# Kernel tuning notes

Hardware: AMD Instinct MI355X
Metric: run time of the kernel (lower is better)

The kernel has to match this reference:

```python
import jax, jax.numpy as jnp
import numpy as np

M, N, P, T = 8000, 63, 64, 5


def setup_inputs() -> dict:
    key = jax.random.key(0)
    ks = jax.random.split(key, 19)
    sn = (1.0 / N) ** 0.5
    sp = (1.0 / P) ** 0.5
    f32 = jnp.float32
    return {
        "A": jax.random.normal(ks[0], (1, M, N), f32),
        "b": jax.random.normal(ks[1], (1, M), f32),
        "c": jax.random.normal(ks[2], (1, N), f32),
        "theta1r": sn * jax.random.normal(ks[3], (P, N + 1), f32),
        "theta1c": sn * jax.random.normal(ks[4], (P, N + 1), f32),
        "theta2rr": sp * jax.random.normal(ks[5], (P, P), f32),
        "theta2rc": sp * jax.random.normal(ks[6], (P, P), f32),
        "theta2cr": sp * jax.random.normal(ks[7], (P, P), f32),
        "theta3rr": sp * jax.random.normal(ks[8], (P, P), f32),
        "theta3rc": sp * jax.random.normal(ks[9], (P, P), f32),
        "theta3cr": sp * jax.random.normal(ks[10], (P, P), f32),
        "theta4rr": sp * jax.random.normal(ks[11], (P,), f32),
        "theta4rc": sp * jax.random.normal(ks[12], (P,), f32),
        "theta4cr": sp * jax.random.normal(ks[13], (P,), f32),
        "theta6r": sp * jax.random.normal(ks[14], (P, P), f32),
        "theta6c": sp * jax.random.normal(ks[15], (P, P), f32),
        "theta7": sp * jax.random.normal(ks[16], (P, P), f32),
        "W8": 0.05 * jax.random.normal(ks[17], (2, 2 * P), f32),
        "b8": 0.05 * jax.random.normal(ks[18], (2,), f32),
        "z": 7,
    }


def reference(A, b, c, theta1r, theta1c, theta2rr, theta2rc, theta2cr,
              theta3rr, theta3rc, theta3cr, theta4rr, theta4rc, theta4cr,
              theta6r, theta6c, theta7, W8, b8, z):
    relu = jax.nn.relu
    m, n = A.shape[1], A.shape[2]
    p = theta1r.shape[0]
    # raw node features: row node v -> [A[v,:], b[v]]; column node m -> [c, 0]
    Fr_raw = jnp.concatenate([A[0], b[0][:, None]], axis=1)        # (m, n+1)
    fc_raw = jnp.concatenate([c[0], jnp.zeros((1,), A.dtype)])     # (n+1,)
    Fr = Fr_raw / jnp.linalg.norm(Fr_raw, axis=1, keepdims=True)   # f(v), v < m
    fc = fc_raw / jnp.linalg.norm(fc_raw)                          # f(m)
    # edge weights w(v,u) = f(v).f(u) are detached in the original (float(...data))
    Frd = jax.lax.stop_gradient(Fr)
    fcd = jax.lax.stop_gradient(fc)
    Wrr = Frd @ Frd.T                                              # (m, m)
    dg = jnp.diagonal(Wrr)
    srr_pos = relu(Wrr).sum(axis=1) - relu(dg)                     # sum over u != v
    srr_neg = relu(-Wrr).sum(axis=1) - relu(-dg)
    wrc = Frd @ fcd                                                # (m,) = w(v, m)
    # identity: sum_u relu(t4 * w_u) = relu(t4) * sum_u relu(w_u) + relu(-t4) * sum_u relu(-w_u)
    Srr = relu(theta4rr)[:, None] * srr_pos[None, :] + relu(-theta4rr)[:, None] * srr_neg[None, :]
    Src = relu(theta4rc)[:, None] * relu(wrc)[None, :] + relu(-theta4rc)[:, None] * relu(-wrc)[None, :]
    scr = relu(theta4cr) * relu(wrc).sum() + relu(-theta4cr) * relu(-wrc).sum()
    edge_r = theta3rr @ Srr + theta3rc @ Src                       # (p, m), constant over t
    edge_c = theta3cr @ scr                                        # (p,)
    fz = Fr[z]                                                     # z < m: row node feature
    t1r = theta1r @ fz                                             # (p,)
    t1c = theta1c @ fz
    # mu init (p, m+1) = [[Ab^T, c0^T]; 0]; split into row columns / column node
    mu_r0 = jnp.zeros((p, m), A.dtype).at[: n + 1].set(Fr_raw.T)
    mu_c0 = jnp.zeros((p,), A.dtype).at[: n + 1].set(fc_raw)

    def step(carry, _):
        mu_r, mu_c = carry
        # row nodes: term2rr uses old mu[:, v]; term2rc uses old mu[:, m]
        new_r = relu(t1r[:, None] + theta2rr @ mu_r + (theta2rc @ mu_c)[:, None] + edge_r)
        # column node updated last within a sweep -> sees updated row embeddings
        new_c = relu(t1c + theta2cr @ new_r.sum(axis=1) + edge_c)
        return (new_r, new_c), None

    (mu_r, mu_c), _ = jax.lax.scan(step, (mu_r0, mu_c0), None, length=T)
    term6 = theta6r @ mu_r.sum(axis=1) + theta6c @ mu_c            # (p,)
    term7 = theta7 @ mu_r[:, z]                                    # (p,)
    feat = jax.nn.sigmoid(jnp.concatenate([term6, term7]))         # (2p,)
    return (feat @ W8.T + b8)[None, :]                             # (1, 2)
```

## Files before the change

### kernel.cpp

```cpp
#include <hip/hip_runtime.h>
#include <math.h>

typedef __attribute__((ext_vector_type(8))) short short8;
typedef __attribute__((ext_vector_type(4))) float f32x4;

#define WS_SPART 0
#define WS_GPART 131072
#define WS_WPART 163840
#define WS_CPART 164864
#define WS_T1R   204864
#define WS_T1C   204928
#define WS_AL    204992
#define WS_BE    205056
#define WS_GA    205120
#define WS_DE    205184
#define WS_ECP   205248
#define WS_ECN   205312
#define WS_W     205376
#define WS_MUZ   205760
#define WS_WSUM  205824
#define WS_RNORM 205888
#define WS_R2H   214080
#define WS_R2L   216128
#define WS_E4    218176
#define WS_FH    250176
#define WS_FL    512320

__device__ __forceinline__ float waveReduceSum(float v) {
#pragma unroll
    for (int m = 32; m >= 1; m >>= 1) v += __shfl_xor(v, m, 64);
    return v;
}
__device__ __forceinline__ unsigned short f2bf(float f) {
    unsigned int u = __float_as_uint(f);
    unsigned int r = (u + 0x7fffu + ((u >> 16) & 1u)) >> 16;
    return (unsigned short)r;
}
__device__ __forceinline__ float bf2f(unsigned short h) {
    return __uint_as_float(((unsigned int)h) << 16);
}

__global__ __launch_bounds__(256) void k_fr(
    const float* __restrict__ A, const float* __restrict__ b, const float* __restrict__ c,
    const float* __restrict__ th1r, const float* __restrict__ th1c,
    const float* __restrict__ th2rr, const float* __restrict__ th2rc,
    const float* __restrict__ th3rr, const float* __restrict__ th3rc, const float* __restrict__ th3cr,
    const float* __restrict__ th4rr, const float* __restrict__ th4rc, const float* __restrict__ th4cr,
    const int* __restrict__ zp,
    unsigned short* __restrict__ Fh, unsigned short* __restrict__ Fl,
    unsigned short* __restrict__ R2H, unsigned short* __restrict__ R2L,
    float* __restrict__ ws)
{
    int tid = threadIdx.x, lane = tid & 63, wid = tid >> 6;

    if (blockIdx.x == 512) {
        __shared__ float fcraw[64], fz[64], sh4a[64], sh4b[64];
        int p = lane;
        int z = zp[0];
        float cv = (p < 63) ? c[p] : 0.f;
        fcraw[p] = cv;
        float av = (p < 63) ? A[z * 63 + p] : b[z];
        float s2 = waveReduceSum(av * av);
        fz[p] = av * rsqrtf(s2);
        __syncthreads();

        float t1 = 0.f, t2 = 0.f, w0 = 0.f;
#pragma unroll 8
        for (int k = 0; k < 64; k++) {
            t1 += th1r[p * 64 + k] * fz[k];
            t2 += th1c[p * 64 + k] * fz[k];
            w0 += th2rc[p * 64 + k] * fcraw[k];
        }
        ws[WS_T1R + p] = t1;
        ws[WS_T1C + p] = t2;
        ws[WS_W + p] = t1 + w0;

        sh4a[p] = th4rr[p];
        sh4b[p] = th4rc[p];
        __syncthreads();
        float a = 0.f, bb = 0.f, g = 0.f, d = 0.f;
#pragma unroll 8
        for (int k = 0; k < 64; k++) {
            float t4 = sh4a[k];
            a  += th3rr[p * 64 + k] * fmaxf(t4, 0.f);
            bb += th3rr[p * 64 + k] * fmaxf(-t4, 0.f);
            float t5 = sh4b[k];
            g  += th3rc[p * 64 + k] * fmaxf(t5, 0.f);
            d  += th3rc[p * 64 + k] * fmaxf(-t5, 0.f);
        }
        ws[WS_AL + p] = a; ws[WS_BE + p] = bb;
        ws[WS_GA + p] = g; ws[WS_DE + p] = d;
        __syncthreads();
        sh4a[p] = th4cr[p];
        __syncthreads();
        float e1 = 0.f, e2 = 0.f;
#pragma unroll 8
        for (int k = 0; k < 64; k++) {
            float t6 = sh4a[k];
            e1 += th3cr[p * 64 + k] * fmaxf(t6, 0.f);
            e2 += th3cr[p * 64 + k] * fmaxf(-t6, 0.f);
        }
        ws[WS_ECP + p] = e1; ws[WS_ECN + p] = e2;

#pragma unroll
        for (int i = 0; i < 16; i++) {
            int idx = tid * 16 + i;
            float f = th2rr[idx];
            unsigned short h = f2bf(f);
            R2H[idx] = h;
            R2L[idx] = f2bf(f - bf2f(h));
        }
        return;
    }

    __shared__ float gsh[64];
    __shared__ float wsh2[2];
    if (tid < 64) gsh[tid] = 0.f;
    if (tid < 2) wsh2[tid] = 0.f;
    __syncthreads();

    float cv = (lane < 63) ? c[lane] : 0.f;
    float cn2 = waveReduceSum(cv * cv);
    float fcnl = cv * rsqrtf(cn2);

    int r0 = blockIdx.x * 16 + wid * 4;
    float gl = 0.f, lp = 0.f, ln = 0.f;
#pragma unroll
    for (int i = 0; i < 4; i++) {
        int r = r0 + i;
        if (r < 8000) {
            float val = (lane < 63) ? A[r * 63 + lane] : b[r];
            float s2 = waveReduceSum(val * val);
            float f = val * rsqrtf(s2);
            unsigned short h = f2bf(f);
            Fh[r * 64 + lane] = h;
            Fl[r * 64 + lane] = f2bf(f - bf2f(h));
            gl += f;
            float w = waveReduceSum(f * fcnl);
            if (lane == 0) {
                ws[WS_RNORM + r] = sqrtf(s2);
                lp += fmaxf(w, 0.f); ln += fmaxf(-w, 0.f);
            }
        } else {
            Fh[r * 64 + lane] = 0;
            Fl[r * 64 + lane] = 0;
        }
    }
    atomicAdd(&gsh[lane], gl);
    if (lane == 0) { atomicAdd(&wsh2[0], lp); atomicAdd(&wsh2[1], ln); }
    __syncthreads();
    if (tid < 64) ws[WS_GPART + blockIdx.x * 64 + tid] = gsh[tid];
    if (tid == 64) ws[WS_WPART + blockIdx.x * 2 + 0] = wsh2[0];
    if (tid == 65) ws[WS_WPART + blockIdx.x * 2 + 1] = wsh2[1];
}

__global__ __launch_bounds__(256) void k_gram(
    const unsigned short* __restrict__ Fh, const unsigned short* __restrict__ Fl,
    float* __restrict__ ws)
{
    __shared__ short BshH[2][16 * 72];
    __shared__ short BshL[2][16 * 72];
    int tid = threadIdx.x, lane = tid & 63, wid = tid >> 6;
    int m = lane & 15, quad = lane >> 4;
    int vbase = blockIdx.x * 256 + wid * 64;
    int sr = tid >> 4, sc = (tid & 15) * 4;

    short8 AH[8], AL[8];
#pragma unroll
    for (int pt = 0; pt < 4; pt++)
#pragma unroll
        for (int q = 0; q < 2; q++) {
            int off = (vbase + pt * 16 + m) * 64 + q * 32 + quad * 8;
            AH[pt * 2 + q] = *(const short8*)(Fh + off);
            AL[pt * 2 + q] = *(const short8*)(Fl + off);
        }
    float srr[16];
#pragma unroll
    for (int i = 0; i < 16; i++) srr[i] = 0.f;

    const int y = blockIdx.y;
    {
        int u0 = y * 16;
        *(uint2*)(&BshH[0][sr * 72 + sc]) = *(const uint2*)(Fh + (u0 + sr) * 64 + sc);
        *(uint2*)(&BshL[0][sr * 72 + sc]) = *(const uint2*)(Fl + (u0 + sr) * 64 + sc);
    }
    __syncthreads();

#pragma unroll 1
    for (int k = 0; k < 32; k++) {
        int cur = k & 1;
        uint2 sH, sL;
        if (k < 31) {
            int u0 = (y + 16 * (k + 1)) * 16;
            sH = *(const uint2*)(Fh + (u0 + sr) * 64 + sc);
            sL = *(const uint2*)(Fl + (u0 + sr) * 64 + sc);
        }
        short8 BH[2], BL[2];
#pragma unroll
        for (int q = 0; q < 2; q++) {
            BH[q] = *(const short8*)(&BshH[cur][m * 72 + q * 32 + quad * 8]);
            BL[q] = *(const short8*)(&BshL[cur][m * 72 + q * 32 + quad * 8]);
        }
#pragma unroll
        for (int pt = 0; pt < 4; pt++) {
            f32x4 a = {0.f, 0.f, 0.f, 0.f};
#pragma unroll
            for (int q = 0; q < 2; q++) {
                a = __builtin_amdgcn_mfma_f32_16x16x32_bf16(AH[pt*2+q], BH[q], a, 0, 0, 0);
                a = __builtin_amdgcn_mfma_f32_16x16x32_bf16(AH[pt*2+q], BL[q], a, 0, 0, 0);
                a = __builtin_amdgcn_mfma_f32_16x16x32_bf16(AL[pt*2+q], BH[q], a, 0, 0, 0);
            }
#pragma unroll
            for (int r = 0; r < 4; r++) srr[pt*4+r] += fmaxf(a[r], 0.f);
        }
        if (k < 31) {
            *(uint2*)(&BshH[1 - cur][sr * 72 + sc]) = sH;
            *(uint2*)(&BshL[1 - cur][sr * 72 + sc]) = sL;
            __syncthreads();
        }
    }
#pragma unroll
    for (int pt = 0; pt < 4; pt++)
#pragma unroll
        for (int r = 0; r < 4; r++) {
            float s = srr[pt * 4 + r];
#pragma unroll
            for (int mm = 8; mm >= 1; mm >>= 1) s += __shfl_xor(s, mm, 64);
            if (m == 0)
                ws[WS_SPART + y * 8192 + vbase + pt * 16 + quad * 4 + r] = s;
        }
}

__global__ __launch_bounds__(256) void k_e4(
    const float* __restrict__ c, float* __restrict__ ws,
    unsigned short* __restrict__ MH, unsigned short* __restrict__ ML)
{
    __shared__ float fcnS[64], gS[64], sprow[64], red[256];
    int tid = threadIdx.x, lane = tid & 63, wid = tid >> 6;

    float cv = (lane < 63) ? c[lane] : 0.f;
    float cn2 = waveReduceSum(cv * cv);
    if (wid == 0) fcnS[lane] = cv * rsqrtf(cn2);

    float gv = 0.f;
    for (int bb = 0; bb < 128; bb++) gv += ws[WS_GPART + (wid * 128 + bb) * 64 + lane];
    red[tid] = gv;
    __syncthreads();
    if (tid < 64) gS[tid] = red[tid] + red[64 + tid] + red[128 + tid] + red[192 + tid];
    if (wid == 1) {
        float wp = 0.f;
#pragma unroll
        for (int k = 0; k < 8; k++) wp += ws[WS_WPART + (lane + 64 * k) * 2];
        wp = waveReduceSum(wp);
        if (lane == 0) ws[WS_WSUM] = wp;
    }
    if (wid == 2) {
        float wn = 0.f;
#pragma unroll
        for (int k = 0; k < 8; k++) wn += ws[WS_WPART + (lane + 64 * k) * 2 + 1];
        wn = waveReduceSum(wn);
        if (lane == 0) ws[WS_WSUM + 1] = wn;
    }
    int v0 = blockIdx.x * 64;
    float sv = 0.f;
#pragma unroll
    for (int y = wid * 4; y < wid * 4 + 4; y++) sv += ws[WS_SPART + y * 8192 + v0 + lane];
    __syncthreads();
    red[tid] = sv;
    __syncthreads();
    if (tid < 64) sprow[tid] = red[tid] + red[64 + tid] + red[128 + tid] + red[192 + tid];
    __syncthreads();

    for (int i2 = 0; i2 < 16; i2++) {
        int i = wid * 16 + i2;
        int v = v0 + i;
        float fr = bf2f(MH[v * 64 + lane]) + bf2f(ML[v * 64 + lane]);
        float dw = waveReduceSum(fr * fcnS[lane]);
        float dg = waveReduceSum(fr * gS[lane]);
        if (lane == 0) {
            float spv = sprow[i];
            float4 e;
            e.x = spv - 1.0f;
            e.y = spv - dg;
            e.z = fmaxf(dw, 0.f);
            e.w = fmaxf(-dw, 0.f);
            *(float4*)(ws + WS_E4 + v * 4) = e;
        }
        float x = fr * ws[WS_RNORM + v];
        unsigned short h = f2bf(x);
        MH[v * 64 + lane] = h;
        ML[v * 64 + lane] = f2bf(x - bf2f(h));
    }
}

__global__ __launch_bounds__(256) void k_mu(
    const int* __restrict__ zp, float* __restrict__ ws,
    unsigned short* __restrict__ MH, unsigned short* __restrict__ ML,
    const unsigned short* __restrict__ R2H, const unsigned short* __restrict__ R2L,
    int t)
{
    __shared__ __align__(16) float wS[64], alS[64], beS[64], gaS[64], deS[64];
    __shared__ float colp[256];
    int tid = threadIdx.x, lane = tid & 63, wid = tid >> 6;
    int m = lane & 15, quad = lane >> 4;
    int v = (blockIdx.x * 4 + wid) * 16 + m;
    int z = zp[0];

    if (wid == 0) wS[lane] = ws[WS_W + t * 64 + lane];
    else if (wid == 1) { alS[lane] = ws[WS_AL + lane]; beS[lane] = ws[WS_BE + lane]; }
    else if (wid == 2) { gaS[lane] = ws[WS_GA + lane]; deS[lane] = ws[WS_DE + lane]; }

    short8 RH[8], RL[8];
#pragma unroll
    for (int pt = 0; pt < 4; pt++)
#pragma unroll
        for (int q = 0; q < 2; q++) {
            int off = (pt * 16 + m) * 64 + q * 32 + quad * 8;
            RH[pt * 2 + q] = *(const short8*)(R2H + off);
            RL[pt * 2 + q] = *(const short8*)(R2L + off);
        }
    short8 BH[2], BL[2];
#pragma unroll
    for (int q = 0; q < 2; q++) {
        BH[q] = *(const short8*)(MH + v * 64 + q * 32 + quad * 8);
        BL[q] = *(const short8*)(ML + v * 64 + q * 32 + quad * 8);
    }
    float4 e = *(const float4*)(ws + WS_E4 + v * 4);
    __syncthreads();

#pragma unroll
    for (int pt = 0; pt < 4; pt++) {
        f32x4 a = {0.f, 0.f, 0.f, 0.f};
#pragma unroll
        for (int q = 0; q < 2; q++) {
            a = __builtin_amdgcn_mfma_f32_16x16x32_bf16(RH[pt*2+q], BH[q], a, 0, 0, 0);
            a = __builtin_amdgcn_mfma_f32_16x16x32_bf16(RH[pt*2+q], BL[q], a, 0, 0, 0);
            a = __builtin_amdgcn_mfma_f32_16x16x32_bf16(RL[pt*2+q], BH[q], a, 0, 0, 0);
        }
        int pbase = pt * 16 + quad * 4;
        float4 w4 = *(const float4*)(wS + pbase);
        float4 a4 = *(const float4*)(alS + pbase);
        float4 b4 = *(const float4*)(beS + pbase);
        float4 g4 = *(const float4*)(gaS + pbase);
        float4 d4 = *(const float4*)(deS + pbase);
        float u0 = fmaxf(a[0] + w4.x + a4.x*e.x + b4.x*e.y + g4.x*e.z + d4.x*e.w, 0.f);
        float u1 = fmaxf(a[1] + w4.y + a4.y*e.x + b4.y*e.y + g4.y*e.z + d4.y*e.w, 0.f);
        float u2 = fmaxf(a[2] + w4.z + a4.z*e.x + b4.z*e.y + g4.z*e.z + d4.z*e.w, 0.f);
        float u3 = fmaxf(a[3] + w4.w + a4.w*e.x + b4.w*e.y + g4.w*e.z + d4.w*e.w, 0.f);
        ushort4 h4, l4;
        h4.x = f2bf(u0); l4.x = f2bf(u0 - bf2f(h4.x));
        h4.y = f2bf(u1); l4.y = f2bf(u1 - bf2f(h4.y));
        h4.z = f2bf(u2); l4.z = f2bf(u2 - bf2f(h4.z));
        h4.w = f2bf(u3); l4.w = f2bf(u3 - bf2f(h4.w));
        *(ushort4*)(MH + v * 64 + pbase) = h4;
        *(ushort4*)(ML + v * 64 + pbase) = l4;
        float c0 = u0, c1 = u1, c2 = u2, c3 = u3;
#pragma unroll
        for (int mm = 1; mm < 16; mm <<= 1) {
            c0 += __shfl_xor(c0, mm, 64);
            c1 += __shfl_xor(c1, mm, 64);
            c2 += __shfl_xor(c2, mm, 64);
            c3 += __shfl_xor(c3, mm, 64);
        }
        if (m == 0) {
            colp[wid * 64 + pbase + 0] = c0;
            colp[wid * 64 + pbase + 1] = c1;
            colp[wid * 64 + pbase + 2] = c2;
            colp[wid * 64 + pbase + 3] = c3;
        }
        if (t == 4 && v == z) {
            float4 o; o.x = u0; o.y = u1; o.z = u2; o.w = u3;
            *(float4*)(ws + WS_MUZ + pbase) = o;
        }
    }
    __syncthreads();
    if (tid < 64)
        ws[WS_CPART + t * 8000 + blockIdx.x * 64 + tid] =
            colp[tid] + colp[64 + tid] + colp[128 + tid] + colp[192 + tid];
}

__global__ __launch_bounds__(256) void k_colup(
    const float* __restrict__ th2cr, const float* __restrict__ th2rc,
    const float* __restrict__ th6r, const float* __restrict__ th6c,
    const float* __restrict__ th7, const float* __restrict__ W8,
    const float* __restrict__ b8,
    float* __restrict__ ws, float* __restrict__ out, int t)
{
    __shared__ float red[256], Ssh[64], ysh[64], wsh[64], feat[128];
    int tid = threadIdx.x, lane = tid & 63, wid = tid >> 6;
    int m = lane & 15, quad = lane >> 4;

    float s = 0.f;
    for (int blk = wid; blk < 125; blk += 4)
        s += ws[WS_CPART + t * 8000 + blk * 64 + lane];
    red[tid] = s;
    __syncthreads();
    if (tid < 64) Ssh[tid] = red[tid] + red[64 + tid] + red[128 + tid] + red[192 + tid];
    __syncthreads();
    {
        int p = wid * 16 + m;
        float acc = 0.f;
        const float4* rowp = (const float4*)(th2cr + p * 64 + quad * 16);
#pragma unroll
        for (int kk = 0; kk < 4; kk++) {
            float4 r4 = rowp[kk];
            acc += r4.x * Ssh[quad * 16 + 4 * kk]     + r4.y * Ssh[quad * 16 + 4 * kk + 1]
                 + r4.z * Ssh[quad * 16 + 4 * kk + 2] + r4.w * Ssh[quad * 16 + 4 * kk + 3];
        }
        acc += __shfl_xor(acc, 16, 64);
        acc += __shfl_xor(acc, 32, 64);
        if (quad == 0)
            ysh[p] = fmaxf(acc + ws[WS_T1C + p] + ws[WS_WSUM] * ws[WS_ECP + p]
                           + ws[WS_WSUM + 1] * ws[WS_ECN + p], 0.f);
    }
    __syncthreads();
    {
        int p = wid * 16 + m;
        float acc = 0.f;
        const float4* rowp = (const float4*)(th2rc + p * 64 + quad * 16);
#pragma unroll
        for (int kk = 0; kk < 4; kk++) {
            float4 r4 = rowp[kk];
            acc += r4.x * ysh[quad * 16 + 4 * kk]     + r4.y * ysh[quad * 16 + 4 * kk + 1]
                 + r4.z * ysh[quad * 16 + 4 * kk + 2] + r4.w * ysh[quad * 16 + 4 * kk + 3];
        }
        acc += __shfl_xor(acc, 16, 64);
        acc += __shfl_xor(acc, 32, 64);
        if (quad == 0) wsh[p] = acc + ws[WS_T1R + p];
    }
    __syncthreads();
    if (tid < 64) ws[WS_W + (t + 1) * 64 + tid] = wsh[tid];

    if (t == 4) {
        int p = tid;
        if (p < 64) {
            float t6 = 0.f, t7 = 0.f;
#pragma unroll 8
            for (int k = 0; k < 64; k++) {
                t6 += th6r[p * 64 + k] * Ssh[k] + th6c[p * 64 + k] * ysh[k];
                t7 += th7[p * 64 + k] * ws[WS_MUZ + k];
            }
            feat[p] = 1.f / (1.f + expf(-t6));
            feat[64 + p] = 1.f / (1.f + expf(-t7));
        }
        __syncthreads();
        if (p < 2) {
            float o = b8[p];
            for (int i = 0; i < 128; i++) o += W8[p * 128 + i] * feat[i];
            out[p] = o;
        }
    }
}

extern "C" void kernel_launch(void* const* d_in, const int* in_sizes, int n_in,
                              void* d_out, int out_size, void* d_ws, size_t ws_size,
                              hipStream_t stream) {
    (void)in_sizes; (void)n_in; (void)out_size; (void)ws_size;
    const float* A     = (const float*)d_in[0];
    const float* b     = (const float*)d_in[1];
    const float* c     = (const float*)d_in[2];
    const float* th1r  = (const float*)d_in[3];
    const float* th1c  = (const float*)d_in[4];
    const float* th2rr = (const float*)d_in[5];
    const float* th2rc = (const float*)d_in[6];
    const float* th2cr = (const float*)d_in[7];
    const float* th3rr = (const float*)d_in[8];
    const float* th3rc = (const float*)d_in[9];
    const float* th3cr = (const float*)d_in[10];
    const float* th4rr = (const float*)d_in[11];
    const float* th4rc = (const float*)d_in[12];
    const float* th4cr = (const float*)d_in[13];
    const float* th6r  = (const float*)d_in[14];
    const float* th6c  = (const float*)d_in[15];
    const float* th7   = (const float*)d_in[16];
    const float* W8    = (const float*)d_in[17];
    const float* b8    = (const float*)d_in[18];
    const int*   zp    = (const int*)d_in[19];
    float* ws  = (float*)d_ws;
    float* out = (float*)d_out;
    unsigned short* Fh  = (unsigned short*)(ws + WS_FH);
    unsigned short* Fl  = (unsigned short*)(ws + WS_FL);
    unsigned short* R2H = (unsigned short*)(ws + WS_R2H);
    unsigned short* R2L = (unsigned short*)(ws + WS_R2L);

    k_fr<<<513, 256, 0, stream>>>(A, b, c, th1r, th1c, th2rr, th2rc, th3rr, th3rc,
                                  th3cr, th4rr, th4rc, th4cr, zp, Fh, Fl, R2H, R2L, ws);
    k_gram<<<dim3(32, 16), 256, 0, stream>>>(Fh, Fl, ws);
    k_e4<<<125, 256, 0, stream>>>(c, ws, Fh, Fl);
    for (int t = 0; t < 5; t++) {
        k_mu<<<125, 256, 0, stream>>>(zp, ws, Fh, Fl, R2H, R2L, t);
        k_colup<<<1, 256, 0, stream>>>(th2cr, th2rc, th6r, th6c, th7, W8, b8, ws, out, t);
    }
}
```

Baseline: 239.0 us.

## Fuse edge prep and all recurrence steps into one persistent kernel with grid sync

```diff
diff --git a/kernel.cpp b/kernel.cpp
--- a/kernel.cpp
+++ b/kernel.cpp
@@ -3,6 +3,8 @@
 
 typedef __attribute__((ext_vector_type(8))) short short8;
 typedef __attribute__((ext_vector_type(4))) float f32x4;
+
+#define NREC 125
 
 #define WS_SPART 0
 #define WS_GPART 131072
@@ -19,12 +21,12 @@
 #define WS_W     205376
 #define WS_MUZ   205760
 #define WS_WSUM  205824
-#define WS_RNORM 205888
-#define WS_R2H   214080
-#define WS_R2L   216128
-#define WS_E4    218176
-#define WS_FH    250176
-#define WS_FL    512320
+#define WS_SYNC  205888
+#define WS_RNORM 205952
+#define WS_R2H   214144
+#define WS_R2L   216192
+#define WS_FH    218240
+#define WS_FL    480384
 
 __device__ __forceinline__ float waveReduceSum(float v) {
 #pragma unroll
@@ -38,6 +40,12 @@
 }
 __device__ __forceinline__ float bf2f(unsigned short h) {
     return __uint_as_float(((unsigned int)h) << 16);
+}
+__device__ __forceinline__ void stG(float* p, float v) {
+    __hip_atomic_store(p, v, __ATOMIC_RELEASE, __HIP_MEMORY_SCOPE_AGENT);
+}
+__device__ __forceinline__ float ldG(const float* p) {
+    return __hip_atomic_load(p, __ATOMIC_ACQUIRE, __HIP_MEMORY_SCOPE_AGENT);
 }
 
 __global__ __launch_bounds__(256) void k_fr(
@@ -57,6 +65,7 @@
         __shared__ float fcraw[64], fz[64], sh4a[64], sh4b[64];
         int p = lane;
         int z = zp[0];
+        if (tid < 16) ((unsigned*)(ws + WS_SYNC))[tid] = 0u;
         float cv = (p < 63) ? c[p] : 0.f;
         fcraw[p] = cv;
         float av = (p < 63) ? A[z * 63 + p] : b[z];
@@ -231,84 +240,107 @@
         }
 }
 
-__global__ __launch_bounds__(256) void k_e4(
-    const float* __restrict__ c, float* __restrict__ ws,
-    unsigned short* __restrict__ MH, unsigned short* __restrict__ ML)
+__global__ __launch_bounds__(256) void k_rec(
+    const float* __restrict__ c,
+    const float* __restrict__ th2cr, const float* __restrict__ th2rc,
+    const float* __restrict__ th6r, const float* __restrict__ th6c,
+    const float* __restrict__ th7, const float* __restrict__ W8,
+    const float* __restrict__ b8, const int* __restrict__ zp,
+    float* __restrict__ ws,
+    const unsigned short* __restrict__ Fh, const unsigned short* __restrict__ Fl,
+    const unsigned short* __restrict__ R2H, const unsigned short* __restrict__ R2L,
+    float* __restrict__ out)
 {
-    __shared__ float fcnS[64], gS[64], sprow[64], red[256];
+    __shared__ float XF[64][68];
+    __shared__ float red[256], colp[256];
+    __shared__ __align__(16) float wS[64], alS[64], beS[64], gaS[64], deS[64];
+    __shared__ float fcnS[64], gS[64], t1rS[64], t1cS[64], ecpS[64], ecnS[64];
+    __shared__ float Ssh[64], ysh[64], wsh[64], wsumS[2], muzS[64], feat[128];
+
     int tid = threadIdx.x, lane = tid & 63, wid = tid >> 6;
-
-    float cv = (lane < 63) ? c[lane] : 0.f;
-    float cn2 = waveReduceSum(cv * cv);
-    if (wid == 0) fcnS[lane] = cv * rsqrtf(cn2);
-
+    int m = lane & 15, quad = lane >> 4;
+    int vblk = blockIdx.x * 64;
+    int cw = wid * 16 + m;
+    int v = vblk + cw;
+    int z = zp[0];
+    unsigned* syncp = (unsigned*)(ws + WS_SYNC);
+
+    if (wid == 0) {
+        float cv = (lane < 63) ? c[lane] : 0.f;
+        float cn2 = waveReduceSum(cv * cv);
+        fcnS[lane] = cv * rsqrtf(cn2);
+        wS[lane] = ws[WS_W + lane];
+    } else if (wid == 1) {
+        alS[lane] = ws[WS_AL + lane]; beS[lane] = ws[WS_BE + lane];
+        t1rS[lane] = ws[WS_T1R + lane];
+        float wp = 0.f;
+#pragma unroll
+        for (int k = 0; k < 8; k++) wp += ws[WS_WPART + (lane + 64 * k) * 2];
+        wp = waveReduceSum(wp);
+        if (lane == 0) wsumS[0] = wp;
+    } else if (wid == 2) {
+        gaS[lane] = ws[WS_GA + lane]; deS[lane] = ws[WS_DE + lane];
+        t1cS[lane] = ws[WS_T1C + lane];
+        float wn = 0.f;
+#pragma unroll
+        for (int k = 0; k < 8; k++) wn += ws[WS_WPART + (lane + 64 * k) * 2 + 1];
+        wn = waveReduceSum(wn);
+        if (lane == 0) wsumS[1] = wn;
+    } else {
+        ecpS[lane] = ws[WS_ECP + lane]; ecnS[lane] = ws[WS_ECN + lane];
+    }
     float gv = 0.f;
     for (int bb = 0; bb < 128; bb++) gv += ws[WS_GPART + (wid * 128 + bb) * 64 + lane];
     red[tid] = gv;
     __syncthreads();
     if (tid < 64) gS[tid] = red[tid] + red[64 + tid] + red[128 + tid] + red[192 + tid];
-    if (wid == 1) {
-        float wp = 0.f;
-#pragma unroll
-        for (int k = 0; k < 8; k++) wp += ws[WS_WPART + (lane + 64 * k) * 2];
-        wp = waveReduceSum(wp);
-        if (lane == 0) ws[WS_WSUM] = wp;
-    }
-    if (wid == 2) {
-        float wn = 0.f;
-#pragma unroll
-        for (int k = 0; k < 8; k++) wn += ws[WS_WPART + (lane + 64 * k) * 2 + 1];
-        wn = waveReduceSum(wn);
-        if (lane == 0) ws[WS_WSUM + 1] = wn;
-    }
-    int v0 = blockIdx.x * 64;
-    float sv = 0.f;
-#pragma unroll
-    for (int y = wid * 4; y < wid * 4 + 4; y++) sv += ws[WS_SPART + y * 8192 + v0 + lane];
     __syncthreads();
-    red[tid] = sv;
-    __syncthreads();
-    if (tid < 64) sprow[tid] = red[tid] + red[64 + tid] + red[128 + tid] + red[192 + tid];
-    __syncthreads();
-
-    for (int i2 = 0; i2 < 16; i2++) {
-        int i = wid * 16 + i2;
-        int v = v0 + i;
-        float fr = bf2f(MH[v * 64 + lane]) + bf2f(ML[v * 64 + lane]);
-        float dw = waveReduceSum(fr * fcnS[lane]);
-        float dg = waveReduceSum(fr * gS[lane]);
-        if (lane == 0) {
-            float spv = sprow[i];
-            float4 e;
-            e.x = spv - 1.0f;
-            e.y = spv - dg;
-            e.z = fmaxf(dw, 0.f);
-            e.w = fmaxf(-dw, 0.f);
-            *(float4*)(ws + WS_E4 + v * 4) = e;
-        }
-        float x = fr * ws[WS_RNORM + v];
-        unsigned short h = f2bf(x);
-        MH[v * 64 + lane] = h;
-        ML[v * 64 + lane] = f2bf(x - bf2f(h));
-    }
-}
-
-__global__ __launch_bounds__(256) void k_mu(
-    const int* __restrict__ zp, float* __restrict__ ws,
-    unsigned short* __restrict__ MH, unsigned short* __restrict__ ML,
-    const unsigned short* __restrict__ R2H, const unsigned short* __restrict__ R2L,
-    int t)
-{
-    __shared__ __align__(16) float wS[64], alS[64], beS[64], gaS[64], deS[64];
-    __shared__ float colp[256];
-    int tid = threadIdx.x, lane = tid & 63, wid = tid >> 6;
-    int m = lane & 15, quad = lane >> 4;
-    int v = (blockIdx.x * 4 + wid) * 16 + m;
-    int z = zp[0];
-
-    if (wid == 0) wS[lane] = ws[WS_W + t * 64 + lane];
-    else if (wid == 1) { alS[lane] = ws[WS_AL + lane]; beS[lane] = ws[WS_BE + lane]; }
-    else if (wid == 2) { gaS[lane] = ws[WS_GA + lane]; deS[lane] = ws[WS_DE + lane]; }
+
+    float x[16];
+#pragma unroll
+    for (int q = 0; q < 2; q++) {
+        short8 h8 = *(const short8*)(Fh + v * 64 + q * 32 + quad * 8);
+        short8 l8 = *(const short8*)(Fl + v * 64 + q * 32 + quad * 8);
+#pragma unroll
+        for (int j = 0; j < 8; j++)
+            x[q * 8 + j] = bf2f((unsigned short)h8[j]) + bf2f((unsigned short)l8[j]);
+    }
+    float dw = 0.f, dg = 0.f;
+#pragma unroll
+    for (int q = 0; q < 2; q++)
+#pragma unroll
+        for (int j = 0; j < 8; j++) {
+            int k = q * 32 + quad * 8 + j;
+            dw += x[q * 8 + j] * fcnS[k];
+            dg += x[q * 8 + j] * gS[k];
+        }
+    dw += __shfl_xor(dw, 16, 64); dw += __shfl_xor(dw, 32, 64);
+    dg += __shfl_xor(dg, 16, 64); dg += __shfl_xor(dg, 32, 64);
+    float spv = 0.f;
+#pragma unroll
+    for (int yy = quad * 4; yy < quad * 4 + 4; yy++)
+        spv += ws[WS_SPART + yy * 8192 + v];
+    spv += __shfl_xor(spv, 16, 64); spv += __shfl_xor(spv, 32, 64);
+    float4 e;
+    e.x = spv - 1.0f;
+    e.y = spv - dg;
+    e.z = fmaxf(dw, 0.f);
+    e.w = fmaxf(-dw, 0.f);
+
+    float rnv = ws[WS_RNORM + v];
+    short8 BH[2], BL[2];
+#pragma unroll
+    for (int q = 0; q < 2; q++) {
+        short8 H, L;
+#pragma unroll
+        for (int j = 0; j < 8; j++) {
+            float xm = x[q * 8 + j] * rnv;
+            unsigned short h = f2bf(xm);
+            H[j] = (short)h;
+            L[j] = (short)f2bf(xm - bf2f(h));
+        }
+        BH[q] = H; BL[q] = L;
+    }
 
     short8 RH[8], RL[8];
 #pragma unroll
@@ -319,135 +351,154 @@
             RH[pt * 2 + q] = *(const short8*)(R2H + off);
             RL[pt * 2 + q] = *(const short8*)(R2L + off);
         }
-    short8 BH[2], BL[2];
-#pragma unroll
-    for (int q = 0; q < 2; q++) {
-        BH[q] = *(const short8*)(MH + v * 64 + q * 32 + quad * 8);
-        BL[q] = *(const short8*)(ML + v * 64 + q * 32 + quad * 8);
-    }
-    float4 e = *(const float4*)(ws + WS_E4 + v * 4);
     __syncthreads();
 
-#pragma unroll
-    for (int pt = 0; pt < 4; pt++) {
-        f32x4 a = {0.f, 0.f, 0.f, 0.f};
-#pragma unroll
-        for (int q = 0; q < 2; q++) {
-            a = __builtin_amdgcn_mfma_f32_16x16x32_bf16(RH[pt*2+q], BH[q], a, 0, 0, 0);
-            a = __builtin_amdgcn_mfma_f32_16x16x32_bf16(RH[pt*2+q], BL[q], a, 0, 0, 0);
-            a = __builtin_amdgcn_mfma_f32_16x16x32_bf16(RL[pt*2+q], BH[q], a, 0, 0, 0);
-        }
-        int pbase = pt * 16 + quad * 4;
-        float4 w4 = *(const float4*)(wS + pbase);
-        float4 a4 = *(const float4*)(alS + pbase);
-        float4 b4 = *(const float4*)(beS + pbase);
-        float4 g4 = *(const float4*)(gaS + pbase);
-        float4 d4 = *(const float4*)(deS + pbase);
-        float u0 = fmaxf(a[0] + w4.x + a4.x*e.x + b4.x*e.y + g4.x*e.z + d4.x*e.w, 0.f);
-        float u1 = fmaxf(a[1] + w4.y + a4.y*e.x + b4.y*e.y + g4.y*e.z + d4.y*e.w, 0.f);
-        float u2 = fmaxf(a[2] + w4.z + a4.z*e.x + b4.z*e.y + g4.z*e.z + d4.z*e.w, 0.f);
-        float u3 = fmaxf(a[3] + w4.w + a4.w*e.x + b4.w*e.y + g4.w*e.z + d4.w*e.w, 0.f);
-        ushort4 h4, l4;
-        h4.x = f2bf(u0); l4.x = f2bf(u0 - bf2f(h4.x));
-        h4.y = f2bf(u1); l4.y = f2bf(u1 - bf2f(h4.y));
-        h4.z = f2bf(u2); l4.z = f2bf(u2 - bf2f(h4.z));
-        h4.w = f2bf(u3); l4.w = f2bf(u3 - bf2f(h4.w));
-        *(ushort4*)(MH + v * 64 + pbase) = h4;
-        *(ushort4*)(ML + v * 64 + pbase) = l4;
-        float c0 = u0, c1 = u1, c2 = u2, c3 = u3;
-#pragma unroll
-        for (int mm = 1; mm < 16; mm <<= 1) {
-            c0 += __shfl_xor(c0, mm, 64);
-            c1 += __shfl_xor(c1, mm, 64);
-            c2 += __shfl_xor(c2, mm, 64);
-            c3 += __shfl_xor(c3, mm, 64);
-        }
-        if (m == 0) {
-            colp[wid * 64 + pbase + 0] = c0;
-            colp[wid * 64 + pbase + 1] = c1;
-            colp[wid * 64 + pbase + 2] = c2;
-            colp[wid * 64 + pbase + 3] = c3;
-        }
-        if (t == 4 && v == z) {
-            float4 o; o.x = u0; o.y = u1; o.z = u2; o.w = u3;
-            *(float4*)(ws + WS_MUZ + pbase) = o;
-        }
-    }
-    __syncthreads();
-    if (tid < 64)
-        ws[WS_CPART + t * 8000 + blockIdx.x * 64 + tid] =
-            colp[tid] + colp[64 + tid] + colp[128 + tid] + colp[192 + tid];
-}
-
-__global__ __launch_bounds__(256) void k_colup(
-    const float* __restrict__ th2cr, const float* __restrict__ th2rc,
-    const float* __restrict__ th6r, const float* __restrict__ th6c,
-    const float* __restrict__ th7, const float* __restrict__ W8,
-    const float* __restrict__ b8,
-    float* __restrict__ ws, float* __restrict__ out, int t)
-{
-    __shared__ float red[256], Ssh[64], ysh[64], wsh[64], feat[128];
-    int tid = threadIdx.x, lane = tid & 63, wid = tid >> 6;
-    int m = lane & 15, quad = lane >> 4;
-
-    float s = 0.f;
-    for (int blk = wid; blk < 125; blk += 4)
-        s += ws[WS_CPART + t * 8000 + blk * 64 + lane];
-    red[tid] = s;
-    __syncthreads();
-    if (tid < 64) Ssh[tid] = red[tid] + red[64 + tid] + red[128 + tid] + red[192 + tid];
-    __syncthreads();
-    {
-        int p = wid * 16 + m;
-        float acc = 0.f;
-        const float4* rowp = (const float4*)(th2cr + p * 64 + quad * 16);
-#pragma unroll
-        for (int kk = 0; kk < 4; kk++) {
-            float4 r4 = rowp[kk];
-            acc += r4.x * Ssh[quad * 16 + 4 * kk]     + r4.y * Ssh[quad * 16 + 4 * kk + 1]
-                 + r4.z * Ssh[quad * 16 + 4 * kk + 2] + r4.w * Ssh[quad * 16 + 4 * kk + 3];
-        }
-        acc += __shfl_xor(acc, 16, 64);
-        acc += __shfl_xor(acc, 32, 64);
-        if (quad == 0)
-            ysh[p] = fmaxf(acc + ws[WS_T1C + p] + ws[WS_WSUM] * ws[WS_ECP + p]
-                           + ws[WS_WSUM + 1] * ws[WS_ECN + p], 0.f);
-    }
-    __syncthreads();
-    {
-        int p = wid * 16 + m;
-        float acc = 0.f;
-        const float4* rowp = (const float4*)(th2rc + p * 64 + quad * 16);
-#pragma unroll
-        for (int kk = 0; kk < 4; kk++) {
-            float4 r4 = rowp[kk];
-            acc += r4.x * ysh[quad * 16 + 4 * kk]     + r4.y * ysh[quad * 16 + 4 * kk + 1]
-                 + r4.z * ysh[quad * 16 + 4 * kk + 2] + r4.w * ysh[quad * 16 + 4 * kk + 3];
-        }
-        acc += __shfl_xor(acc, 16, 64);
-        acc += __shfl_xor(acc, 32, 64);
-        if (quad == 0) wsh[p] = acc + ws[WS_T1R + p];
-    }
-    __syncthreads();
-    if (tid < 64) ws[WS_W + (t + 1) * 64 + tid] = wsh[tid];
-
-    if (t == 4) {
-        int p = tid;
-        if (p < 64) {
-            float t6 = 0.f, t7 = 0.f;
+    for (int t = 0; t < 5; t++) {
+#pragma unroll
+        for (int pt = 0; pt < 4; pt++) {
+            f32x4 a = {0.f, 0.f, 0.f, 0.f};
+#pragma unroll
+            for (int q = 0; q < 2; q++) {
+                a = __builtin_amdgcn_mfma_f32_16x16x32_bf16(RH[pt*2+q], BH[q], a, 0, 0, 0);
+                a = __builtin_amdgcn_mfma_f32_16x16x32_bf16(RH[pt*2+q], BL[q], a, 0, 0, 0);
+                a = __builtin_amdgcn_mfma_f32_16x16x32_bf16(RL[pt*2+q], BH[q], a, 0, 0, 0);
+            }
+            int pbase = pt * 16 + quad * 4;
+            float4 w4 = *(const float4*)(wS + pbase);
+            float4 a4 = *(const float4*)(alS + pbase);
+            float4 b4 = *(const float4*)(beS + pbase);
+            float4 g4 = *(const float4*)(gaS + pbase);
+            float4 d4 = *(const float4*)(deS + pbase);
+            float u0 = fmaxf(a[0] + w4.x + a4.x*e.x + b4.x*e.y + g4.x*e.z + d4.x*e.w, 0.f);
+            float u1 = fmaxf(a[1] + w4.y + a4.y*e.x + b4.y*e.y + g4.y*e.z + d4.y*e.w, 0.f);
+            float u2 = fmaxf(a[2] + w4.z + a4.z*e.x + b4.z*e.y + g4.z*e.z + d4.z*e.w, 0.f);
+            float u3 = fmaxf(a[3] + w4.w + a4.w*e.x + b4.w*e.y + g4.w*e.z + d4.w*e.w, 0.f);
+            float4 uf; uf.x = u0; uf.y = u1; uf.z = u2; uf.w = u3;
+            *(float4*)(&XF[cw][pbase]) = uf;
+            float c0 = u0, c1 = u1, c2 = u2, c3 = u3;
+#pragma unroll
+            for (int mm = 1; mm < 16; mm <<= 1) {
+                c0 += __shfl_xor(c0, mm, 64);
+                c1 += __shfl_xor(c1, mm, 64);
+                c2 += __shfl_xor(c2, mm, 64);
+                c3 += __shfl_xor(c3, mm, 64);
+            }
+            if (m == 0) {
+                colp[wid * 64 + pbase + 0] = c0;
+                colp[wid * 64 + pbase + 1] = c1;
+                colp[wid * 64 + pbase + 2] = c2;
+                colp[wid * 64 + pbase + 3] = c3;
+            }
+            if (t == 4 && v == z) {
+                stG(ws + WS_MUZ + pbase + 0, u0);
+                stG(ws + WS_MUZ + pbase + 1, u1);
+                stG(ws + WS_MUZ + pbase + 2, u2);
+                stG(ws + WS_MUZ + pbase + 3, u3);
+            }
+        }
+        __syncthreads();
+        if (tid < 64)
+            stG(ws + WS_CPART + t * 8000 + blockIdx.x * 64 + tid,
+                colp[tid] + colp[64 + tid] + colp[128 + tid] + colp[192 + tid]);
+        if (t < 4) {
+#pragma unroll
+            for (int q = 0; q < 2; q++) {
+                float4 f0 = *(const float4*)(&XF[cw][q * 32 + quad * 8]);
+                float4 f1 = *(const float4*)(&XF[cw][q * 32 + quad * 8 + 4]);
+                float xv[8] = {f0.x, f0.y, f0.z, f0.w, f1.x, f1.y, f1.z, f1.w};
+                short8 H, L;
+#pragma unroll
+                for (int j = 0; j < 8; j++) {
+                    unsigned short h = f2bf(xv[j]);
+                    H[j] = (short)h;
+                    L[j] = (short)f2bf(xv[j] - bf2f(h));
+                }
+                BH[q] = H; BL[q] = L;
+            }
+        }
+        __syncthreads();
+        if (tid == 0)
+            __hip_atomic_fetch_add(&syncp[t], 1u, __ATOMIC_ACQ_REL, __HIP_MEMORY_SCOPE_AGENT);
+
+        if (blockIdx.x == 0) {
+            if (tid == 0) {
+                while (__hip_atomic_load(&syncp[t], __ATOMIC_ACQUIRE, __HIP_MEMORY_SCOPE_AGENT) < NREC)
+                    __builtin_amdgcn_s_sleep(2);
+            }
+            __syncthreads();
+            float s = 0.f;
+            for (int blk = wid; blk < NREC; blk += 4)
+                s += ldG(ws + WS_CPART + t * 8000 + blk * 64 + lane);
+            red[tid] = s;
+            __syncthreads();
+            if (tid < 64) Ssh[tid] = red[tid] + red[64 + tid] + red[128 + tid] + red[192 + tid];
+            __syncthreads();
+            {
+                int p = wid * 16 + m;
+                float acc = 0.f;
+                const float4* rowp = (const float4*)(th2cr + p * 64 + quad * 16);
+#pragma unroll
+                for (int kk = 0; kk < 4; kk++) {
+                    float4 r4 = rowp[kk];
+                    acc += r4.x * Ssh[quad * 16 + 4 * kk]     + r4.y * Ssh[quad * 16 + 4 * kk + 1]
+                         + r4.z * Ssh[quad * 16 + 4 * kk + 2] + r4.w * Ssh[quad * 16 + 4 * kk + 3];
+                }
+                acc += __shfl_xor(acc, 16, 64);
+                acc += __shfl_xor(acc, 32, 64);
+                if (quad == 0)
+                    ysh[p] = fmaxf(acc + t1cS[p] + wsumS[0] * ecpS[p] + wsumS[1] * ecnS[p], 0.f);
+            }
+            __syncthreads();
+            if (t < 4) {
+                {
+                    int p = wid * 16 + m;
+                    float acc = 0.f;
+                    const float4* rowp = (const float4*)(th2rc + p * 64 + quad * 16);
+#pragma unroll
+                    for (int kk = 0; kk < 4; kk++) {
+                        float4 r4 = rowp[kk];
+                        acc += r4.x * ysh[quad * 16 + 4 * kk]     + r4.y * ysh[quad * 16 + 4 * kk + 1]
+                             + r4.z * ysh[quad * 16 + 4 * kk + 2] + r4.w * ysh[quad * 16 + 4 * kk + 3];
+                    }
+                    acc += __shfl_xor(acc, 16, 64);
+                    acc += __shfl_xor(acc, 32, 64);
+                    if (quad == 0) wsh[p] = acc + t1rS[p];
+                }
+                __syncthreads();
+                if (tid < 64) stG(ws + WS_W + (t + 1) * 64 + tid, wsh[tid]);
+                __syncthreads();
+                if (tid == 0)
+                    __hip_atomic_store(&syncp[8 + t], 1u, __ATOMIC_RELEASE, __HIP_MEMORY_SCOPE_AGENT);
+            } else {
+                if (tid < 64) muzS[tid] = ldG(ws + WS_MUZ + tid);
+                __syncthreads();
+                int p = tid;
+                if (p < 64) {
+                    float t6 = 0.f, t7 = 0.f;
 #pragma unroll 8
-            for (int k = 0; k < 64; k++) {
-                t6 += th6r[p * 64 + k] * Ssh[k] + th6c[p * 64 + k] * ysh[k];
-                t7 += th7[p * 64 + k] * ws[WS_MUZ + k];
-            }
-            feat[p] = 1.f / (1.f + expf(-t6));
-            feat[64 + p] = 1.f / (1.f + expf(-t7));
-        }
-        __syncthreads();
-        if (p < 2) {
-            float o = b8[p];
-            for (int i = 0; i < 128; i++) o += W8[p * 128 + i] * feat[i];
-            out[p] = o;
+                    for (int k = 0; k < 64; k++) {
+                        t6 += th6r[p * 64 + k] * Ssh[k] + th6c[p * 64 + k] * ysh[k];
+                        t7 += th7[p * 64 + k] * muzS[k];
+                    }
+                    feat[p] = 1.f / (1.f + expf(-t6));
+                    feat[64 + p] = 1.f / (1.f + expf(-t7));
+                }
+                __syncthreads();
+                if (p < 2) {
+                    float o = b8[p];
+                    for (int i = 0; i < 128; i++) o += W8[p * 128 + i] * feat[i];
+                    out[p] = o;
+                }
+            }
+        }
+        if (t < 4) {
+            if (tid == 0) {
+                while (__hip_atomic_load(&syncp[8 + t], __ATOMIC_ACQUIRE, __HIP_MEMORY_SCOPE_AGENT) == 0u)
+                    __builtin_amdgcn_s_sleep(2);
+            }
+            __syncthreads();
+            if (tid < 64) wS[tid] = ldG(ws + WS_W + (t + 1) * 64 + tid);
+            __syncthreads();
         }
     }
 }
@@ -486,9 +537,6 @@
     k_fr<<<513, 256, 0, stream>>>(A, b, c, th1r, th1c, th2rr, th2rc, th3rr, th3rc,
                                   th3cr, th4rr, th4rc, th4cr, zp, Fh, Fl, R2H, R2L, ws);
     k_gram<<<dim3(32, 16), 256, 0, stream>>>(Fh, Fl, ws);
-    k_e4<<<125, 256, 0, stream>>>(c, ws, Fh, Fl);
-    for (int t = 0; t < 5; t++) {
-        k_mu<<<125, 256, 0, stream>>>(zp, ws, Fh, Fl, R2H, R2L, t);
-        k_colup<<<1, 256, 0, stream>>>(th2cr, th2rc, th6r, th6c, th7, W8, b8, ws, out, t);
-    }
-}
+    k_rec<<<NREC, 256, 0, stream>>>(c, th2cr, th2rc, th6r, th6c, th7, W8, b8, zp,
+                                    ws, Fh, Fl, R2H, R2L, out);
+}
```

After: 632.0 us. 2.64x slower.

## Exploit Gram matrix symmetry with triangular tile grid in relu row-sum kernel

Applied to the files above, without the earlier changes.

```diff
diff --git a/kernel.cpp b/kernel.cpp
--- a/kernel.cpp
+++ b/kernel.cpp
@@ -5,26 +5,26 @@
 typedef __attribute__((ext_vector_type(4))) float f32x4;
 
 #define WS_SPART 0
-#define WS_GPART 131072
-#define WS_WPART 163840
-#define WS_CPART 164864
-#define WS_T1R   204864
-#define WS_T1C   204928
-#define WS_AL    204992
-#define WS_BE    205056
-#define WS_GA    205120
-#define WS_DE    205184
-#define WS_ECP   205248
-#define WS_ECN   205312
-#define WS_W     205376
-#define WS_MUZ   205760
-#define WS_WSUM  205824
-#define WS_RNORM 205888
-#define WS_R2H   214080
-#define WS_R2L   216128
-#define WS_E4    218176
-#define WS_FH    250176
-#define WS_FL    512320
+#define WS_GPART 1048576
+#define WS_WPART 1081344
+#define WS_CPART 1082368
+#define WS_T1R   1122368
+#define WS_T1C   1122432
+#define WS_AL    1122496
+#define WS_BE    1122560
+#define WS_GA    1122624
+#define WS_DE    1122688
+#define WS_ECP   1122752
+#define WS_ECN   1122816
+#define WS_W     1122880
+#define WS_MUZ   1123264
+#define WS_WSUM  1123328
+#define WS_RNORM 1123392
+#define WS_R2H   1131584
+#define WS_R2L   1133632
+#define WS_E4    1135680
+#define WS_FH    1167680
+#define WS_FL    1429824
 
 __device__ __forceinline__ float waveReduceSum(float v) {
 #pragma unroll
@@ -158,77 +158,70 @@
     const unsigned short* __restrict__ Fh, const unsigned short* __restrict__ Fl,
     float* __restrict__ ws)
 {
-    __shared__ short BshH[2][16 * 72];
-    __shared__ short BshL[2][16 * 72];
+    __shared__ float rowb[64];
+    __shared__ float colb[4][64];
     int tid = threadIdx.x, lane = tid & 63, wid = tid >> 6;
     int m = lane & 15, quad = lane >> 4;
-    int vbase = blockIdx.x * 256 + wid * 64;
-    int sr = tid >> 4, sc = (tid & 15) * 4;
-
-    short8 AH[8], AL[8];
-#pragma unroll
-    for (int pt = 0; pt < 4; pt++)
+
+    int bx = blockIdx.x;
+    int j = (int)((sqrtf(8.0f * (float)bx + 1.0f) - 1.0f) * 0.5f);
+    while ((j + 1) * (j + 2) / 2 <= bx) j++;
+    while (j * (j + 1) / 2 > bx) j--;
+    int i = bx - j * (j + 1) / 2;
+
+    short8 AH[2], AL[2];
+#pragma unroll
+    for (int q = 0; q < 2; q++) {
+        int off = (i * 64 + wid * 16 + m) * 64 + q * 32 + quad * 8;
+        AH[q] = *(const short8*)(Fh + off);
+        AL[q] = *(const short8*)(Fl + off);
+    }
+    short8 BH[4][2], BL[4][2];
+#pragma unroll
+    for (int s = 0; s < 4; s++)
 #pragma unroll
         for (int q = 0; q < 2; q++) {
-            int off = (vbase + pt * 16 + m) * 64 + q * 32 + quad * 8;
-            AH[pt * 2 + q] = *(const short8*)(Fh + off);
-            AL[pt * 2 + q] = *(const short8*)(Fl + off);
-        }
-    float srr[16];
-#pragma unroll
-    for (int i = 0; i < 16; i++) srr[i] = 0.f;
-
-    const int y = blockIdx.y;
-    {
-        int u0 = y * 16;
-        *(uint2*)(&BshH[0][sr * 72 + sc]) = *(const uint2*)(Fh + (u0 + sr) * 64 + sc);
-        *(uint2*)(&BshL[0][sr * 72 + sc]) = *(const uint2*)(Fl + (u0 + sr) * 64 + sc);
-    }
-    __syncthreads();
-
-#pragma unroll 1
-    for (int k = 0; k < 32; k++) {
-        int cur = k & 1;
-        uint2 sH, sL;
-        if (k < 31) {
-            int u0 = (y + 16 * (k + 1)) * 16;
-            sH = *(const uint2*)(Fh + (u0 + sr) * 64 + sc);
-            sL = *(const uint2*)(Fl + (u0 + sr) * 64 + sc);
-        }
-        short8 BH[2], BL[2];
+            int off = (j * 64 + s * 16 + m) * 64 + q * 32 + quad * 8;
+            BH[s][q] = *(const short8*)(Fh + off);
+            BL[s][q] = *(const short8*)(Fl + off);
+        }
+
+    float rs[4] = {0.f, 0.f, 0.f, 0.f};
+    float cs[4];
+#pragma unroll
+    for (int s = 0; s < 4; s++) {
+        f32x4 a = {0.f, 0.f, 0.f, 0.f};
 #pragma unroll
         for (int q = 0; q < 2; q++) {
-            BH[q] = *(const short8*)(&BshH[cur][m * 72 + q * 32 + quad * 8]);
-            BL[q] = *(const short8*)(&BshL[cur][m * 72 + q * 32 + quad * 8]);
-        }
-#pragma unroll
-        for (int pt = 0; pt < 4; pt++) {
-            f32x4 a = {0.f, 0.f, 0.f, 0.f};
-#pragma unroll
-            for (int q = 0; q < 2; q++) {
-                a = __builtin_amdgcn_mfma_f32_16x16x32_bf16(AH[pt*2+q], BH[q], a, 0, 0, 0);
-                a = __builtin_amdgcn_mfma_f32_16x16x32_bf16(AH[pt*2+q], BL[q], a, 0, 0, 0);
-                a = __builtin_amdgcn_mfma_f32_16x16x32_bf16(AL[pt*2+q], BH[q], a, 0, 0, 0);
-            }
-#pragma unroll
-            for (int r = 0; r < 4; r++) srr[pt*4+r] += fmaxf(a[r], 0.f);
-        }
-        if (k < 31) {
-            *(uint2*)(&BshH[1 - cur][sr * 72 + sc]) = sH;
-            *(uint2*)(&BshL[1 - cur][sr * 72 + sc]) = sL;
-            __syncthreads();
-        }
-    }
-#pragma unroll
-    for (int pt = 0; pt < 4; pt++)
-#pragma unroll
-        for (int r = 0; r < 4; r++) {
-            float s = srr[pt * 4 + r];
-#pragma unroll
-            for (int mm = 8; mm >= 1; mm >>= 1) s += __shfl_xor(s, mm, 64);
-            if (m == 0)
-                ws[WS_SPART + y * 8192 + vbase + pt * 16 + quad * 4 + r] = s;
-        }
+            a = __builtin_amdgcn_mfma_f32_16x16x32_bf16(AH[q], BH[s][q], a, 0, 0, 0);
+            a = __builtin_amdgcn_mfma_f32_16x16x32_bf16(AH[q], BL[s][q], a, 0, 0, 0);
+            a = __builtin_amdgcn_mfma_f32_16x16x32_bf16(AL[q], BH[s][q], a, 0, 0, 0);
+        }
+        float c0 = fmaxf(a[0], 0.f), c1 = fmaxf(a[1], 0.f);
+        float c2 = fmaxf(a[2], 0.f), c3 = fmaxf(a[3], 0.f);
+        rs[0] += c0; rs[1] += c1; rs[2] += c2; rs[3] += c3;
+        cs[s] = c0 + c1 + c2 + c3;
+    }
+#pragma unroll
+    for (int r = 0; r < 4; r++) {
+        float s = rs[r];
+        s += __shfl_xor(s, 1, 64); s += __shfl_xor(s, 2, 64);
+        s += __shfl_xor(s, 4, 64); s += __shfl_xor(s, 8, 64);
+        if (m == 0) rowb[wid * 16 + quad * 4 + r] = s;
+    }
+#pragma unroll
+    for (int s = 0; s < 4; s++) {
+        float v = cs[s];
+        v += __shfl_xor(v, 16, 64); v += __shfl_xor(v, 32, 64);
+        if (quad == 0) colb[wid][s * 16 + m] = v;
+    }
+    __syncthreads();
+    if (tid < 64) {
+        ws[WS_SPART + j * 8192 + i * 64 + tid] = rowb[tid];
+        if (i < j)
+            ws[WS_SPART + i * 8192 + j * 64 + tid] =
+                colb[0][tid] + colb[1][tid] + colb[2][tid] + colb[3][tid];
+    }
 }
 
 __global__ __launch_bounds__(256) void k_e4(
@@ -263,8 +256,8 @@
     }
     int v0 = blockIdx.x * 64;
     float sv = 0.f;
-#pragma unroll
-    for (int y = wid * 4; y < wid * 4 + 4; y++) sv += ws[WS_SPART + y * 8192 + v0 + lane];
+    for (int k = wid * 32; k < wid * 32 + 32; k++)
+        sv += ws[WS_SPART + k * 8192 + v0 + lane];
     __syncthreads();
     red[tid] = sv;
     __syncthreads();
@@ -485,7 +478,7 @@
 
     k_fr<<<513, 256, 0, stream>>>(A, b, c, th1r, th1c, th2rr, th2rc, th3rr, th3rc,
                                   th3cr, th4rr, th4rc, th4cr, zp, Fh, Fl, R2H, R2L, ws);
-    k_gram<<<dim3(32, 16), 256, 0, stream>>>(Fh, Fl, ws);
+    k_gram<<<8256, 256, 0, stream>>>(Fh, Fl, ws);
     k_e4<<<125, 256, 0, stream>>>(c, ws, Fh, Fl);
     for (int t = 0; t < 5; t++) {
         k_mu<<<125, 256, 0, stream>>>(zp, ws, Fh, Fl, R2H, R2L, t);
```

Result: slower. 285.5 us (+19.4%).
